# Kernel tuning notes

Measured on AMD Instinct MI355X. Metric: run time of the kernel, lower is better.

The kernel has to match this reference:

```python
import jax, jax.numpy as jnp
import numpy as np

C_LIGHT = 1.0
CHUNK = 363  # 35937 = 99 * 363 spatial modes per scan step


def _spatial_mode_sum(r, spatial_kernel):
    # sum_n spatial_kernel[n] * sin(n * r), reduced over modes in chunks so we
    # never materialize the full [N, 35937] sin table.
    M = spatial_kernel.shape[0]
    nn = jnp.arange(M, dtype=r.dtype).reshape(-1, CHUNK)      # [steps, CHUNK]
    kk = spatial_kernel.reshape(-1, CHUNK)                    # [steps, CHUNK]

    def body(acc, nk):
        n_c, k_c = nk
        # [N, CHUNK] @ [CHUNK] -> [N]
        return acc + jnp.sin(r[:, None] * n_c[None, :]) @ k_c, None

    acc, _ = jax.lax.scan(body, jnp.zeros_like(r), (nn, kk))
    return acc


def setup_inputs() -> dict:
    key = jax.random.key(0)
    k1, k2, k3 = jax.random.split(key, 3)
    N = 131072
    M_SPATIAL = 35937   # (2*16+1)**3
    M_TEMPORAL = 33     # 2*16+1
    return {
        "spacetime_coords": jax.random.normal(k1, (N, 4), jnp.float32) * 2.0,
        "spatial_kernel": jax.random.normal(k2, (M_SPATIAL,), jnp.float32) * 0.1,
        "temporal_kernel": jax.random.normal(k3, (M_TEMPORAL,), jnp.float32) * 0.1,
        "mass_parameter": jnp.float32(1.0),
        "coupling_strength": jnp.float32(0.1),
    }


def reference(spacetime_coords, spatial_kernel, temporal_kernel,
              mass_parameter, coupling_strength):
    t = spacetime_coords[..., 0]
    x = spacetime_coords[..., 1]
    y = spacetime_coords[..., 2]
    z = spacetime_coords[..., 3]

    spatial_distance_sq = x * x + y * y + z * z
    temporal_distance_sq = (C_LIGHT * t) ** 2
    interval = temporal_distance_sq - spatial_distance_sq

    timelike = interval > 0
    lightlike = jnp.abs(interval) < 1e-10

    # Retarded Green function on the forward timelike region
    spatial_distance = jnp.sqrt(spatial_distance_sq + 1e-12)
    green = jnp.where(
        timelike & (t > 0),
        coupling_strength * jnp.exp(-mass_parameter * spatial_distance) / spatial_distance,
        jnp.zeros_like(t),
    )
    # enforce_causality mask (timelike | lightlike)
    kernel_values = jnp.where(timelike | lightlike, green, jnp.zeros_like(green))

    # Spatial component: sum_n k_n * sin(n*r) / (r + 1e-6); division factored out
    r = jnp.sqrt(spatial_distance_sq + 1e-12)
    spatial_component = _spatial_mode_sum(r, spatial_kernel) / (r + 1e-6)

    # Temporal component: sum_n k_n * cos((n+1)*0.1 * t) * exp(-0.1*|t|)
    freqs = (jnp.arange(temporal_kernel.shape[0], dtype=t.dtype) + 1.0) * 0.1
    envelope = jnp.exp(-0.1 * jnp.abs(t))
    temporal_component = (jnp.cos(t[:, None] * freqs[None, :]) @ temporal_kernel) * envelope

    total_kernel = kernel_values + spatial_component * temporal_component

    # Future light-cone causality mask
    future_lightcone = (temporal_distance_sq >= spatial_distance_sq) & (t >= 0)
    return jnp.where(future_lightcone, total_kernel, jnp.zeros_like(total_kernel))
```

## Files before the change

### kernel.cpp

```cpp
#include <hip/hip_runtime.h>
#include <math.h>


constexpr int NCHUNK = 64;
constexpr int CH     = 576;
constexpr int MPAD   = NCHUNK * CH + 64;

__global__ __launch_bounds__(256)
void mask_kernel(const float4* __restrict__ coords,
                 const float* __restrict__ massp,
                 const float* __restrict__ coupp,
                 const float* __restrict__ tk,
                 const float* __restrict__ ksp,
                 float* __restrict__ out,
                 int* __restrict__ counter,
                 int* __restrict__ list,
                 float* __restrict__ fw,
                 float* __restrict__ rw,
                 float* __restrict__ kpad,
                 int N, int M, int MT)
{
    int i = blockIdx.x * blockDim.x + threadIdx.x;

    if (i < MPAD) kpad[i] = (i < M) ? ksp[i] : 0.0f;
    if (i >= N) return;

    float4 c = coords[i];
    float t = c.x;
    float rsq = c.y * c.y + c.z * c.z + c.w * c.w;
    float t2  = t * t;
    bool  fl  = (t2 >= rsq) && (t >= 0.0f);
    float r   = sqrtf(rsq + 1e-12f);
    float g   = 0.0f;
    if (fl && (t2 > rsq) && (t > 0.0f))
        g = (*coupp) * __expf(-(*massp) * r) / r;
    out[i] = fl ? g : 0.0f;

    unsigned long long bal = __ballot(fl);
    if (fl) {
        float tb = 0.1f * t;
        float T  = 0.0f;
        for (int m = 1; m <= MT; ++m)
            T = fmaf(tk[m - 1], __cosf(tb * (float)m), T);
        T *= __expf(-0.1f * fabsf(t));
        float f = T / (r + 1e-6f);

        int lane   = threadIdx.x & 63;
        int prefix = __popcll(bal & ((1ull << lane) - 1ull));
        int base   = 0;
        if (prefix == 0)
            base = atomicAdd(counter, __popcll(bal));
        int first = __ffsll(bal) - 1;
        base = __shfl(base, first);
        int pos = base + prefix;
        list[pos] = i;
        fw[pos]   = f;
        rw[pos]   = r;
    }
}

__global__ __launch_bounds__(256)
void mode_kernel(const float* __restrict__ kpad,
                 float* __restrict__ out,
                 const int* __restrict__ counter,
                 const int* __restrict__ list,
                 const float* __restrict__ fw,
                 const float* __restrict__ rw)
{
    int gtid   = blockIdx.x * blockDim.x + threadIdx.x;
    int wave   = gtid >> 6;
    int lane   = threadIdx.x & 63;
    int nwaves = (gridDim.x * blockDim.x) >> 6;

    int count   = __builtin_amdgcn_readfirstlane(*counter);
    int ngroups = (count + 63) >> 6;
    int items   = ngroups * NCHUNK;

    for (int it = wave; it < items; it += nwaves) {
        int group = __builtin_amdgcn_readfirstlane(it >> 6);
        int chunk = __builtin_amdgcn_readfirstlane(it & (NCHUNK - 1));
        int li    = group * 64 + lane;

        bool  act = (li < count);
        int   idx = 0;
        float r = 0.0f, f = 0.0f;
        if (act) { idx = list[li]; r = rw[li]; f = fw[li]; }

        int n0 = chunk * CH;

        double y = (double)n0 * (double)r;
        double q = rint(y * 0.15915494309189535);
        float  base = (float)(y - q * 6.283185307179586);

        float t2c = 2.0f * __cosf(8.0f * r);

        float sc[8], sp[8], acc[8];
#pragma unroll
        for (int j = 0; j < 8; ++j) {
            sc[j]  = __sinf(fmaf((float)j,       r, base));
            sp[j]  = __sinf(fmaf((float)(j - 8), r, base));
            acc[j] = 0.0f;
        }

        const float* kc = kpad + n0;
        float4 cA = *(const float4*)(kc);
        float4 cB = *(const float4*)(kc + 4);
        float4 cC = *(const float4*)(kc + 8);
        float4 cD = *(const float4*)(kc + 12);

        constexpr int DSTEPS = CH / 16;
        for (int s = 0; s < DSTEPS; ++s) {
            const float* kn = kc + 16 * (s + 1);
            float4 nA = *(const float4*)(kn);
            float4 nB = *(const float4*)(kn + 4);
            float4 nC = *(const float4*)(kn + 8);
            float4 nD = *(const float4*)(kn + 12);

            float kv0[8] = {cA.x, cA.y, cA.z, cA.w, cB.x, cB.y, cB.z, cB.w};
            float kv1[8] = {cC.x, cC.y, cC.z, cC.w, cD.x, cD.y, cD.z, cD.w};
#pragma unroll
            for (int j = 0; j < 8; ++j) {
                acc[j] = fmaf(kv0[j], sc[j], acc[j]);
                sp[j]  = fmaf(t2c, sc[j], -sp[j]);
            }
#pragma unroll
            for (int j = 0; j < 8; ++j) {
                acc[j] = fmaf(kv1[j], sp[j], acc[j]);
                sc[j]  = fmaf(t2c, sp[j], -sc[j]);
            }
            cA = nA; cB = nB; cC = nC; cD = nD;
        }

        float S = ((acc[0] + acc[1]) + (acc[2] + acc[3])) +
                  ((acc[4] + acc[5]) + (acc[6] + acc[7]));
        if (act)
            atomicAdd(&out[idx], S * f);
    }
}

__global__ __launch_bounds__(256)
void fallback_kernel(const float4* __restrict__ coords,
                     const float* __restrict__ ksp,
                     const float* __restrict__ tk,
                     const float* __restrict__ massp,
                     const float* __restrict__ coupp,
                     float* __restrict__ out, int N, int M, int MT)
{
    int i = blockIdx.x * blockDim.x + threadIdx.x;
    if (i >= N) return;
    float4 c = coords[i];
    float t = c.x;
    float rsq = c.y * c.y + c.z * c.z + c.w * c.w;
    float t2 = t * t;
    bool fl = (t2 >= rsq) && (t >= 0.0f);
    if (!fl) { out[i] = 0.0f; return; }
    float r = sqrtf(rsq + 1e-12f);
    float g = 0.0f;
    if ((t2 > rsq) && (t > 0.0f)) g = (*coupp) * __expf(-(*massp) * r) / r;
    float T = 0.0f, tb = 0.1f * t;
    for (int m = 1; m <= MT; ++m) T = fmaf(tk[m - 1], __cosf(tb * (float)m), T);
    T *= __expf(-0.1f * fabsf(t));
    float f = T / (r + 1e-6f);
    float S = 0.0f;
    for (int n0 = 0; n0 < M; n0 += 1024) {
        int nh = min(n0 + 1024, M);
        double y = (double)n0 * (double)r;
        double q = rint(y * 0.15915494309189535);
        float base = (float)(y - q * 6.283185307179586);
        float s0 = __sinf(base - r), s1 = __sinf(base);
        float tc = 2.0f * __cosf(r);
        for (int n = n0; n < nh; ++n) {
            S = fmaf(ksp[n], s1, S);
            float nx = fmaf(tc, s1, -s0);
            s0 = s1; s1 = nx;
        }
    }
    out[i] = g + S * f;
}

extern "C" void kernel_launch(void* const* d_in, const int* in_sizes, int n_in,
                              void* d_out, int out_size, void* d_ws, size_t ws_size,
                              hipStream_t stream)
{
    const float4* coords = (const float4*)d_in[0];
    const float*  ksp    = (const float*)d_in[1];
    const float*  tk     = (const float*)d_in[2];
    const float*  massp  = (const float*)d_in[3];
    const float*  coupp  = (const float*)d_in[4];
    float*        out    = (float*)d_out;

    int N  = in_sizes[0] / 4;
    int M  = in_sizes[1];
    int MT = in_sizes[2];

    size_t off_list = 16;
    size_t off_fw   = off_list + (size_t)N * 4;
    size_t off_rw   = off_fw   + (size_t)N * 4;
    size_t off_k    = off_rw   + (size_t)N * 4;
    size_t needed   = off_k    + (size_t)MPAD * 4;

    if (ws_size < needed || M > NCHUNK * CH) {
        fallback_kernel<<<(N + 255) / 256, 256, 0, stream>>>(
            coords, ksp, tk, massp, coupp, out, N, M, MT);
        return;
    }

    int*   counter = (int*)d_ws;
    int*   list    = (int*)((char*)d_ws + off_list);
    float* fw      = (float*)((char*)d_ws + off_fw);
    float* rw      = (float*)((char*)d_ws + off_rw);
    float* kpad    = (float*)((char*)d_ws + off_k);

    hipMemsetAsync(d_ws, 0, 16, stream);

    int nthreads = (N > MPAD) ? N : MPAD;
    mask_kernel<<<(nthreads + 255) / 256, 256, 0, stream>>>(
        coords, massp, coupp, tk, ksp, out, counter, list, fw, rw, kpad, N, M, MT);

    mode_kernel<<<2048, 256, 0, stream>>>(kpad, out, counter, list, fw, rw);
}
```

Before: 123.7 us.

## Stage mode-kernel coefficients in per-wave LDS with double-buffered prefetch

The mode kernel now copies each chunk's spatial-kernel coefficients into a per-wave shared-memory buffer with coalesced float4 loads. It also prefetches the next work item's point data and coefficients into registers while computing the current item, then writes them into the alternate buffer. The aim is to replace the wave-uniform global scalar/vector loads inside the inner recurrence loop with LDS broadcast reads and to hide global latency. It adds LDS usage (about 18 KB per block), which may reduce occupancy, and relies on the wave-local buffer without explicit barriers.

```diff
diff --git a/kernel.cpp b/kernel.cpp
--- a/kernel.cpp
+++ b/kernel.cpp
@@ -67,32 +67,57 @@
                  const float* __restrict__ fw,
                  const float* __restrict__ rw)
 {
+    __shared__ float smem[4][2][CH];
+
     int gtid   = blockIdx.x * blockDim.x + threadIdx.x;
     int wave   = gtid >> 6;
     int lane   = threadIdx.x & 63;
+    int wb     = (threadIdx.x >> 6) & 3;
     int nwaves = (gridDim.x * blockDim.x) >> 6;
 
     int count   = __builtin_amdgcn_readfirstlane(*counter);
     int ngroups = (count + 63) >> 6;
     int items   = ngroups * NCHUNK;
 
-    for (int it = wave; it < items; it += nwaves) {
-        int group = __builtin_amdgcn_readfirstlane(it >> 6);
-        int chunk = __builtin_amdgcn_readfirstlane(it & (NCHUNK - 1));
-        int li    = group * 64 + lane;
-
-        bool  act = (li < count);
-        int   idx = 0;
-        float r = 0.0f, f = 0.0f;
-        if (act) { idx = list[li]; r = rw[li]; f = fw[li]; }
+    int it = wave;
+    if (it >= items) return;
+
+    int chunk = it & (NCHUNK - 1);
+    int li    = (it >> 6) * 64 + lane;
+    int   idx = 0; float r = 0.0f, f = 0.0f;
+    if (li < count) { idx = list[li]; r = rw[li]; f = fw[li]; }
+    {
+        const float4* kc = (const float4*)(kpad + chunk * CH);
+        float4 g0 = kc[lane];
+        float4 g1 = kc[lane + 64];
+        float4 g2 = make_float4(0.f, 0.f, 0.f, 0.f);
+        if (lane < 16) g2 = kc[lane + 128];
+        float4* dst = (float4*)&smem[wb][0][0];
+        dst[lane] = g0; dst[lane + 64] = g1;
+        if (lane < 16) dst[lane + 128] = g2;
+    }
+    int cur = 0;
+
+    while (true) {
+        int  itn  = it + nwaves;
+        bool last = (itn >= items);
+        int  itp  = last ? it : itn;
+
+        int chunkn = itp & (NCHUNK - 1);
+        int lin    = (itp >> 6) * 64 + lane;
+        int   idxn = 0; float rn = 0.0f, fn = 0.0f;
+        if (lin < count) { idxn = list[lin]; rn = rw[lin]; fn = fw[lin]; }
+        const float4* kcn = (const float4*)(kpad + chunkn * CH);
+        float4 h0 = kcn[lane];
+        float4 h1 = kcn[lane + 64];
+        float4 h2 = make_float4(0.f, 0.f, 0.f, 0.f);
+        if (lane < 16) h2 = kcn[lane + 128];
 
         int n0 = chunk * CH;
-
         double y = (double)n0 * (double)r;
         double q = rint(y * 0.15915494309189535);
         float  base = (float)(y - q * 6.283185307179586);
-
-        float t2c = 2.0f * __cosf(8.0f * r);
+        float  t2c  = 2.0f * __cosf(8.0f * r);
 
         float sc[8], sp[8], acc[8];
 #pragma unroll
@@ -102,22 +127,16 @@
             acc[j] = 0.0f;
         }
 
-        const float* kc = kpad + n0;
-        float4 cA = *(const float4*)(kc);
-        float4 cB = *(const float4*)(kc + 4);
-        float4 cC = *(const float4*)(kc + 8);
-        float4 cD = *(const float4*)(kc + 12);
-
-        constexpr int DSTEPS = CH / 16;
-        for (int s = 0; s < DSTEPS; ++s) {
-            const float* kn = kc + 16 * (s + 1);
-            float4 nA = *(const float4*)(kn);
-            float4 nB = *(const float4*)(kn + 4);
-            float4 nC = *(const float4*)(kn + 8);
-            float4 nD = *(const float4*)(kn + 12);
-
-            float kv0[8] = {cA.x, cA.y, cA.z, cA.w, cB.x, cB.y, cB.z, cB.w};
-            float kv1[8] = {cC.x, cC.y, cC.z, cC.w, cD.x, cD.y, cD.z, cD.w};
+        const float4* lk = (const float4*)&smem[wb][cur][0];
+        for (int s2 = 0; s2 < 18; ++s2) {
+            float4 q0 = lk[8 * s2 + 0], q1 = lk[8 * s2 + 1];
+            float4 q2 = lk[8 * s2 + 2], q3 = lk[8 * s2 + 3];
+            float4 q4 = lk[8 * s2 + 4], q5 = lk[8 * s2 + 5];
+            float4 q6 = lk[8 * s2 + 6], q7 = lk[8 * s2 + 7];
+            float kv0[8] = {q0.x, q0.y, q0.z, q0.w, q1.x, q1.y, q1.z, q1.w};
+            float kv1[8] = {q2.x, q2.y, q2.z, q2.w, q3.x, q3.y, q3.z, q3.w};
+            float kv2[8] = {q4.x, q4.y, q4.z, q4.w, q5.x, q5.y, q5.z, q5.w};
+            float kv3[8] = {q6.x, q6.y, q6.z, q6.w, q7.x, q7.y, q7.z, q7.w};
 #pragma unroll
             for (int j = 0; j < 8; ++j) {
                 acc[j] = fmaf(kv0[j], sc[j], acc[j]);
@@ -128,13 +147,32 @@
                 acc[j] = fmaf(kv1[j], sp[j], acc[j]);
                 sc[j]  = fmaf(t2c, sp[j], -sc[j]);
             }
-            cA = nA; cB = nB; cC = nC; cD = nD;
+#pragma unroll
+            for (int j = 0; j < 8; ++j) {
+                acc[j] = fmaf(kv2[j], sc[j], acc[j]);
+                sp[j]  = fmaf(t2c, sc[j], -sp[j]);
+            }
+#pragma unroll
+            for (int j = 0; j < 8; ++j) {
+                acc[j] = fmaf(kv3[j], sp[j], acc[j]);
+                sc[j]  = fmaf(t2c, sp[j], -sc[j]);
+            }
+        }
+
+        {
+            float4* dst = (float4*)&smem[wb][cur ^ 1][0];
+            dst[lane] = h0; dst[lane + 64] = h1;
+            if (lane < 16) dst[lane + 128] = h2;
         }
 
         float S = ((acc[0] + acc[1]) + (acc[2] + acc[3])) +
                   ((acc[4] + acc[5]) + (acc[6] + acc[7]));
-        if (act)
+        if (li < count)
             atomicAdd(&out[idx], S * f);
+
+        if (last) break;
+        it = itn; chunk = chunkn; li = lin;
+        idx = idxn; r = rn; f = fn; cur ^= 1;
     }
 }
 
```

After: 203.9 us. 64.9% more time.

## Assign mode chunks to blocks and stage chunk coefficients in shared memory

Applied to the files above, without the earlier changes.

The mode-sum kernel now uses a fixed grid of blocks per mode chunk instead of a grid-stride loop over (group, chunk) work items. Each block stages its 576-coefficient chunk into LDS and reads it from there, with the inner loop manually double-buffered. The point list is loaded before the barrier so that load latency overlaps the staging. This trades uniform global/scalar coefficient loads for LDS reads and a fixed work mapping, which can leave waves unbalanced when the group count does not divide evenly. The fallback path now also triggers for small N.

```diff
diff --git a/kernel.cpp b/kernel.cpp
--- a/kernel.cpp
+++ b/kernel.cpp
@@ -5,6 +5,8 @@
 constexpr int NCHUNK = 64;
 constexpr int CH     = 576;
 constexpr int MPAD   = NCHUNK * CH + 64;
+constexpr int BPC    = 47;
+constexpr int ITERS  = 18;
 
 __global__ __launch_bounds__(256)
 void mask_kernel(const float4* __restrict__ coords,
@@ -67,68 +69,85 @@
                  const float* __restrict__ fw,
                  const float* __restrict__ rw)
 {
-    int gtid   = blockIdx.x * blockDim.x + threadIdx.x;
-    int wave   = gtid >> 6;
-    int lane   = threadIdx.x & 63;
-    int nwaves = (gridDim.x * blockDim.x) >> 6;
-
-    int count   = __builtin_amdgcn_readfirstlane(*counter);
+    __shared__ float kch[CH + 32];
+
+    int tid   = threadIdx.x;
+    int lane  = tid & 63;
+    int w     = tid >> 6;
+    int chunk = __builtin_amdgcn_readfirstlane(blockIdx.x / BPC);
+    int lb    = blockIdx.x - chunk * BPC;
+    int g0    = lb * 4 + w;
+
+    int   li  = g0 * 64 + lane;
+    int   idx = list[li];
+    float r   = rw[li];
+    float f   = fw[li];
+    int   cnt = *counter;
+
+    if (tid < (CH + 32) / 4)
+        ((float4*)kch)[tid] = ((const float4*)(kpad + chunk * CH))[tid];
+    __syncthreads();
+
+    int count   = __builtin_amdgcn_readfirstlane(cnt);
     int ngroups = (count + 63) >> 6;
-    int items   = ngroups * NCHUNK;
-
-    for (int it = wave; it < items; it += nwaves) {
-        int group = __builtin_amdgcn_readfirstlane(it >> 6);
-        int chunk = __builtin_amdgcn_readfirstlane(it & (NCHUNK - 1));
-        int li    = group * 64 + lane;
-
-        bool  act = (li < count);
-        int   idx = 0;
-        float r = 0.0f, f = 0.0f;
-        if (act) { idx = list[li]; r = rw[li]; f = fw[li]; }
-
-        int n0 = chunk * CH;
+    int n0      = chunk * CH;
+
+    for (int g = g0; g < ngroups; g += BPC * 4) {
+        if (g != g0) {
+            li = g * 64 + lane;
+            idx = list[li]; r = rw[li]; f = fw[li];
+        }
+        bool act = (li < count);
 
         double y = (double)n0 * (double)r;
-        double q = rint(y * 0.15915494309189535);
-        float  base = (float)(y - q * 6.283185307179586);
-
-        float t2c = 2.0f * __cosf(8.0f * r);
+        float  b = (float)(y - rint(y * 0.15915494309189535) * 6.283185307179586);
+        float  t2c = 2.0f * __cosf(8.0f * r);
 
         float sc[8], sp[8], acc[8];
 #pragma unroll
         for (int j = 0; j < 8; ++j) {
-            sc[j]  = __sinf(fmaf((float)j,       r, base));
-            sp[j]  = __sinf(fmaf((float)(j - 8), r, base));
+            sc[j]  = __sinf(fmaf((float)j,       r, b));
+            sp[j]  = __sinf(fmaf((float)(j - 8), r, b));
             acc[j] = 0.0f;
         }
 
-        const float* kc = kpad + n0;
-        float4 cA = *(const float4*)(kc);
-        float4 cB = *(const float4*)(kc + 4);
-        float4 cC = *(const float4*)(kc + 8);
-        float4 cD = *(const float4*)(kc + 12);
-
-        constexpr int DSTEPS = CH / 16;
-        for (int s = 0; s < DSTEPS; ++s) {
-            const float* kn = kc + 16 * (s + 1);
-            float4 nA = *(const float4*)(kn);
-            float4 nB = *(const float4*)(kn + 4);
-            float4 nC = *(const float4*)(kn + 8);
-            float4 nD = *(const float4*)(kn + 12);
-
-            float kv0[8] = {cA.x, cA.y, cA.z, cA.w, cB.x, cB.y, cB.z, cB.w};
-            float kv1[8] = {cC.x, cC.y, cC.z, cC.w, cD.x, cD.y, cD.z, cD.w};
-#pragma unroll
-            for (int j = 0; j < 8; ++j) {
-                acc[j] = fmaf(kv0[j], sc[j], acc[j]);
-                sp[j]  = fmaf(t2c, sc[j], -sp[j]);
+        const float4* lk = (const float4*)kch;
+        float4 kA = lk[0], kB = lk[1], kC = lk[2], kD = lk[3];
+
+#pragma unroll 1
+        for (int s = 0; s < ITERS; ++s) {
+            float4 mA = lk[8 * s + 4], mB = lk[8 * s + 5];
+            float4 mC = lk[8 * s + 6], mD = lk[8 * s + 7];
+            {
+                float kv0[8] = {kA.x, kA.y, kA.z, kA.w, kB.x, kB.y, kB.z, kB.w};
+                float kv1[8] = {kC.x, kC.y, kC.z, kC.w, kD.x, kD.y, kD.z, kD.w};
+#pragma unroll
+                for (int j = 0; j < 8; ++j) {
+                    acc[j] = fmaf(kv0[j], sc[j], acc[j]);
+                    sp[j]  = fmaf(t2c, sc[j], -sp[j]);
+                }
+#pragma unroll
+                for (int j = 0; j < 8; ++j) {
+                    acc[j] = fmaf(kv1[j], sp[j], acc[j]);
+                    sc[j]  = fmaf(t2c, sp[j], -sc[j]);
+                }
             }
-#pragma unroll
-            for (int j = 0; j < 8; ++j) {
-                acc[j] = fmaf(kv1[j], sp[j], acc[j]);
-                sc[j]  = fmaf(t2c, sp[j], -sc[j]);
+            kA = lk[8 * s + 8];  kB = lk[8 * s + 9];
+            kC = lk[8 * s + 10]; kD = lk[8 * s + 11];
+            {
+                float kv0[8] = {mA.x, mA.y, mA.z, mA.w, mB.x, mB.y, mB.z, mB.w};
+                float kv1[8] = {mC.x, mC.y, mC.z, mC.w, mD.x, mD.y, mD.z, mD.w};
+#pragma unroll
+                for (int j = 0; j < 8; ++j) {
+                    acc[j] = fmaf(kv0[j], sc[j], acc[j]);
+                    sp[j]  = fmaf(t2c, sc[j], -sp[j]);
+                }
+#pragma unroll
+                for (int j = 0; j < 8; ++j) {
+                    acc[j] = fmaf(kv1[j], sp[j], acc[j]);
+                    sc[j]  = fmaf(t2c, sp[j], -sc[j]);
+                }
             }
-            cA = nA; cB = nB; cC = nC; cD = nD;
         }
 
         float S = ((acc[0] + acc[1]) + (acc[2] + acc[3])) +
@@ -199,7 +218,7 @@
     size_t off_k    = off_rw   + (size_t)N * 4;
     size_t needed   = off_k    + (size_t)MPAD * 4;
 
-    if (ws_size < needed || M > NCHUNK * CH) {
+    if (ws_size < needed || M > NCHUNK * CH || N < NCHUNK * BPC * 8) {
         fallback_kernel<<<(N + 255) / 256, 256, 0, stream>>>(
             coords, ksp, tk, massp, coupp, out, N, M, MT);
         return;
@@ -217,5 +236,5 @@
     mask_kernel<<<(nthreads + 255) / 256, 256, 0, stream>>>(
         coords, massp, coupp, tk, ksp, out, counter, list, fw, rw, kpad, N, M, MT);
 
-    mode_kernel<<<2048, 256, 0, stream>>>(kpad, out, counter, list, fw, rw);
-}
+    mode_kernel<<<NCHUNK * BPC, 256, 0, stream>>>(kpad, out, counter, list, fw, rw);
+}
```

Result: faster. 118.5 us (-4.2%).
